# Kernel tuning notes

Measured on AMD Instinct MI355X. Metric: run time of the kernel, lower is better.

Reference implementation:

```python
import jax, jax.numpy as jnp
import numpy as np

EMBED = 1024
HEADS = 16
HEAD_DIM = EMBED // HEADS
B, S = 2, 2048


def setup_inputs() -> dict:
    key = jax.random.key(0)
    ks = jax.random.split(key, 11)
    sc = 1.0 / np.sqrt(EMBED)
    d = {
        'query': jax.random.normal(ks[0], (B, S, EMBED), jnp.float32),
        'key':   jax.random.normal(ks[1], (B, S, EMBED), jnp.float32),
        'value': jax.random.normal(ks[2], (B, S, EMBED), jnp.float32),
        'Wq': jax.random.normal(ks[3], (EMBED, EMBED), jnp.float32) * sc,
        'bq': jnp.zeros((EMBED,), jnp.float32),
        'Wk': jax.random.normal(ks[4], (EMBED, EMBED), jnp.float32) * sc,
        'bk': jnp.zeros((EMBED,), jnp.float32),
        'Wv': jax.random.normal(ks[5], (EMBED, EMBED), jnp.float32) * sc,
        'bv': jnp.zeros((EMBED,), jnp.float32),
        'Wo': jax.random.normal(ks[6], (EMBED, EMBED), jnp.float32) * sc,
        'bo': jnp.zeros((EMBED,), jnp.float32),
    }
    return d


def _split_heads(x):
    b, s, _ = x.shape
    return x.reshape(b, s, HEADS, HEAD_DIM).transpose(0, 2, 1, 3)  # [B,H,S,D]


def reference(query, key, value, Wq, bq, Wk, bk, Wv, bv, Wo, bo):
    # nn.Linear: y = x @ W^T + b
    q = _split_heads(query @ Wq.T + bq)
    k = _split_heads(key @ Wk.T + bk)
    v = _split_heads(value @ Wv.T + bv)
    scale = 1.0 / np.sqrt(HEAD_DIM).astype(np.float32)
    attn = jnp.einsum('bhqd,bhkd->bhqk', q, k) * scale  # [B,H,S,S]
    attn = jax.nn.softmax(attn, axis=-1)
    out = jnp.einsum('bhqk,bhkd->bhqd', attn, v)
    out = out.transpose(0, 2, 1, 3).reshape(query.shape[0], -1, EMBED)
    return out @ Wo.T + bo
```

## Files before the change

### kernel.cpp

```cpp
#include <hip/hip_runtime.h>

typedef _Float16 f16;
typedef __fp16   fp16n2 __attribute__((ext_vector_type(2)));
typedef _Float16 f16x8 __attribute__((ext_vector_type(8)));
typedef float    f32x2 __attribute__((ext_vector_type(2)));
typedef float    f32x4 __attribute__((ext_vector_type(4)));
typedef float    f32x16 __attribute__((ext_vector_type(16)));
typedef int      i32x2 __attribute__((ext_vector_type(2)));
typedef unsigned short u16;
typedef unsigned long long u64;

#define B_ 2
#define S_ 2048
#define E_ 1024
#define H_ 16
#define D_ 64
#define M_ (B_*S_)
#define LOG2E 1.44269504088896340736f

__device__ __forceinline__ f32x4 mfma16(f16x8 a, f16x8 b, f32x4 c) {
  return __builtin_amdgcn_mfma_f32_16x16x32_f16(a, b, c, 0, 0, 0);
}
__device__ __forceinline__ f32x16 mfma32(f16x8 a, f16x8 b, f32x16 c) {
  return __builtin_amdgcn_mfma_f32_32x32x16_f16(a, b, c, 0, 0, 0);
}

__device__ __forceinline__ void gload_lds16(const void* g, void* l) {
  __builtin_amdgcn_global_load_lds(
      (const __attribute__((address_space(1))) unsigned int*)g,
      (__attribute__((address_space(3))) unsigned int*)l, 16, 0, 0);
}

__device__ __forceinline__ int pkrtz(float a, float b) {
  union { fp16n2 h; int i; } u;
  u.h = __builtin_amdgcn_cvt_pkrtz(a, b);
  return u.i;
}

__device__ __forceinline__ u16 f16bits(float x) {
  union { f16 h; u16 u; } c; c.h = (f16)x; return c.u;
}

__device__ __forceinline__ f32x16 Z16() {
  f32x16 z = {0.f,0.f,0.f,0.f,0.f,0.f,0.f,0.f,0.f,0.f,0.f,0.f,0.f,0.f,0.f,0.f};
  return z;
}

__device__ __forceinline__ f32x2 pr2(const f32x16& v, int j) {
  return (f32x2){v[2 * j], v[2 * j + 1]};
}

__global__ __launch_bounds__(256) void cast_all(
    const float* __restrict__ q, const float* __restrict__ k, const float* __restrict__ v,
    const float* __restrict__ wq, const float* __restrict__ wk,
    const float* __restrict__ wv, const float* __restrict__ wo,
    f16* __restrict__ xq, f16* __restrict__ xk, f16* __restrict__ xv,
    f16* __restrict__ wqh, f16* __restrict__ wkh, f16* __restrict__ wvh,
    f16* __restrict__ woh) {
  int i = blockIdx.x * 256 + threadIdx.x;
  const float* src; f16* dst; int off;
  if (i < 3 * 524288) {
    int seg = i >> 19; off = i & 524287;
    src = seg == 0 ? q : seg == 1 ? k : v;
    dst = seg == 0 ? xq : seg == 1 ? xk : xv;
  } else {
    int j = i - 3 * 524288;
    int seg = j >> 17; off = j & 131071;
    src = seg == 0 ? wq : seg == 1 ? wk : seg == 2 ? wv : wo;
    dst = seg == 0 ? wqh : seg == 1 ? wkh : seg == 2 ? wvh : woh;
  }
  const float4* s = (const float4*)src;
  float4 a = s[off * 2], b = s[off * 2 + 1];
  f16x8 o = { (f16)a.x, (f16)a.y, (f16)a.z, (f16)a.w,
              (f16)b.x, (f16)b.y, (f16)b.z, (f16)b.w };
  *(f16x8*)&dst[(size_t)off * 8] = o;
}

__device__ __forceinline__ void gemm_core128(const f16* __restrict__ A,
                                             const f16* __restrict__ Bm,
                                             int m0, int n0,
                                             f32x4 (&acc)[4][2]) {
  __shared__ f16 Al[2][128 * 32];
  __shared__ f16 Bl[2][128 * 32];
  const int tid = threadIdx.x;
  const int w = tid >> 6, lane = tid & 63, lg = lane >> 4, ll = lane & 15;
  const int wr = (w & 1) * 64, wc = (w >> 1) * 32;

  const f32x4 zero4 = {0.f, 0.f, 0.f, 0.f};
#pragma unroll
  for (int m = 0; m < 4; ++m) { acc[m][0] = zero4; acc[m][1] = zero4; }

  const int lgs = (lg ^ ((ll >> 1) & 3)) * 8;
  const int row = tid >> 2;
  const int c8  = ((tid & 3) ^ ((tid >> 3) & 3)) * 8;

  for (int k0 = 0; k0 < 1024; k0 += 64) {
    __syncthreads();
#pragma unroll
    for (int ks = 0; ks < 2; ++ks) {
      gload_lds16(&A [(size_t)(m0 + row) * 1024 + k0 + ks * 32 + c8], &Al[ks][tid * 8]);
      gload_lds16(&Bm[(size_t)(n0 + row) * 1024 + k0 + ks * 32 + c8], &Bl[ks][tid * 8]);
    }
    __syncthreads();

#pragma unroll
    for (int ks = 0; ks < 2; ++ks) {
      f16x8 af[4], bf[2];
#pragma unroll
      for (int m = 0; m < 4; ++m) af[m] = *(const f16x8*)&Al[ks][(wr + m * 16 + ll) * 32 + lgs];
#pragma unroll
      for (int n = 0; n < 2; ++n) bf[n] = *(const f16x8*)&Bl[ks][(wc + n * 16 + ll) * 32 + lgs];
#pragma unroll
      for (int m = 0; m < 4; ++m)
#pragma unroll
        for (int n = 0; n < 2; ++n) acc[m][n] = mfma16(af[m], bf[n], acc[m][n]);
    }
  }
}

__global__ __launch_bounds__(512, 4) void gemm_qkv(
    const f16* __restrict__ Xq, const f16* __restrict__ Xk, const f16* __restrict__ Xv,
    const f16* __restrict__ Wq, const f16* __restrict__ Wk, const f16* __restrict__ Wv,
    const float* __restrict__ bq, const float* __restrict__ bk, const float* __restrict__ bv,
    f16* __restrict__ Qb, f16* __restrict__ Kb, f16* __restrict__ Vt) {
  const int z = blockIdx.z;
  const f16*   A    = (z == 0) ? Xq : (z == 1) ? Xk : Xv;
  const f16*   Bm   = (z == 0) ? Wq : (z == 1) ? Wk : Wv;
  const float* bias = (z == 0) ? bq : (z == 1) ? bk : bv;
  const float scale = (z == 0) ? (0.125f * LOG2E) : 1.0f;
  const int m0 = blockIdx.x * 128, n0 = blockIdx.y * 128;

  f32x4 acc[4][2];
  gemm_core128(A, Bm, m0, n0, acc);

  const int tid = threadIdx.x;
  const int w = tid >> 6, lane = tid & 63, lg = lane >> 4, ll = lane & 15;
  const int wr = (w & 1) * 64, wc = (w >> 1) * 32;

  if (z == 2) {
#pragma unroll
    for (int m = 0; m < 4; ++m)
#pragma unroll
      for (int n = 0; n < 2; ++n) {
        int col = n0 + wc + n * 16 + ll;
        float bv_ = bias[col];
        int h = col >> 6, d = col & 63;
        int rowb = m0 + wr + m * 16 + lg * 4;
        int b = rowb >> 11, s = rowb & 2047;
        u64 pk = (u64)f16bits(acc[m][n][0] + bv_)
               | ((u64)f16bits(acc[m][n][1] + bv_) << 16)
               | ((u64)f16bits(acc[m][n][2] + bv_) << 32)
               | ((u64)f16bits(acc[m][n][3] + bv_) << 48);
        *(u64*)&Vt[(((size_t)(b * H_ + h)) * D_ + d) * S_ + s] = pk;
      }
    return;
  }

  f16* dst = (z == 0) ? Qb : Kb;
#pragma unroll
  for (int m = 0; m < 4; ++m)
#pragma unroll
    for (int n = 0; n < 2; ++n) {
      int col = n0 + wc + n * 16 + ll;
      float bv_ = bias[col];
      int h = col >> 6, d = col & 63;
#pragma unroll
      for (int r = 0; r < 4; ++r) {
        int row = m0 + wr + m * 16 + lg * 4 + r;
        int b = row >> 11, s = row & 2047;
        float v = (acc[m][n][r] + bv_) * scale;
        dst[(((size_t)(b * H_ + h)) * S_ + s) * D_ + d] = (f16)v;
      }
    }
}

__device__ __forceinline__ void gemm_core64(const f16* __restrict__ A,
                                            const f16* __restrict__ Bm,
                                            int m0, int n0,
                                            f32x4 (&acc)[4][2]) {
  __shared__ f16 Al[2][128 * 32];
  __shared__ f16 Bl[2][64 * 32];
  const int tid = threadIdx.x;
  const int w = tid >> 6, lane = tid & 63, lg = lane >> 4, ll = lane & 15;
  const int wr = (w >> 1) * 64, wc = (w & 1) * 32;

  const f32x4 zero4 = {0.f, 0.f, 0.f, 0.f};
#pragma unroll
  for (int m = 0; m < 4; ++m) { acc[m][0] = zero4; acc[m][1] = zero4; }

  const int lgs = (lg ^ ((ll >> 1) & 3)) * 8;

  for (int k0 = 0; k0 < 1024; k0 += 64) {
    __syncthreads();
#pragma unroll
    for (int ks = 0; ks < 2; ++ks) {
#pragma unroll
      for (int it = 0; it < 2; ++it) {
        int chunk = it * 256 + tid;
        int row = chunk >> 2;
        int c8 = ((chunk & 3) ^ ((chunk >> 3) & 3)) * 8;
        gload_lds16(&A[(size_t)(m0 + row) * 1024 + k0 + ks * 32 + c8],
                    &Al[ks][chunk * 8]);
      }
      {
        int chunk = tid;
        int row = chunk >> 2;
        int c8 = ((chunk & 3) ^ ((chunk >> 3) & 3)) * 8;
        gload_lds16(&Bm[(size_t)(n0 + row) * 1024 + k0 + ks * 32 + c8],
                    &Bl[ks][chunk * 8]);
      }
    }
    __syncthreads();

#pragma unroll
    for (int ks = 0; ks < 2; ++ks) {
      f16x8 af[4], bf[2];
#pragma unroll
      for (int m = 0; m < 4; ++m) af[m] = *(const f16x8*)&Al[ks][(wr + m * 16 + ll) * 32 + lgs];
#pragma unroll
      for (int n = 0; n < 2; ++n) bf[n] = *(const f16x8*)&Bl[ks][(wc + n * 16 + ll) * 32 + lgs];
#pragma unroll
      for (int m = 0; m < 4; ++m)
#pragma unroll
        for (int n = 0; n < 2; ++n) acc[m][n] = mfma16(af[m], bf[n], acc[m][n]);
    }
  }
}

__global__ __launch_bounds__(256) void gemm_out(const f16* __restrict__ A,
                                                const f16* __restrict__ W,
                                                const float* __restrict__ bias,
                                                float* __restrict__ out) {
  const int m0 = blockIdx.x * 128, n0 = blockIdx.y * 64;
  f32x4 acc[4][2];
  gemm_core64(A, W, m0, n0, acc);

  const int tid = threadIdx.x;
  const int w = tid >> 6, lane = tid & 63, lg = lane >> 4, ll = lane & 15;
  const int wr = (w >> 1) * 64, wc = (w & 1) * 32;
#pragma unroll
  for (int m = 0; m < 4; ++m)
#pragma unroll
    for (int n = 0; n < 2; ++n) {
      int col = n0 + wc + n * 16 + ll;
      float bv_ = bias[col];
#pragma unroll
      for (int r = 0; r < 4; ++r) {
        int row = m0 + wr + m * 16 + lg * 4 + r;
        out[(size_t)row * 1024 + col] = acc[m][n][r] + bv_;
      }
    }
}

__global__ __launch_bounds__(512, 4) void attn_fwd(const f16* __restrict__ Q,
                                                   const f16* __restrict__ K,
                                                   const f16* __restrict__ VT,
                                                   f16* __restrict__ O) {
  const int qt = blockIdx.x, bh = blockIdx.y;
  const int tid = threadIdx.x;
  const int w = tid >> 6, lane = tid & 63;
  const int ql = lane & 31, hi = lane >> 5;
  const int qsub = w & 3, kvh = w >> 2;

  __shared__ __align__(16) char smem[32768];
  char* hb = smem + kvh * 16384;

  const f16* Qb = Q  + (size_t)bh * S_ * D_;
  const f16* Kb = K  + (size_t)bh * S_ * D_ + (size_t)(kvh * 1024) * D_;
  const f16* Vb = VT + (size_t)bh * D_ * S_ + kvh * 1024;
  const int q0 = qt * 128 + qsub * 32;

  f16x8 qf[4];
#pragma unroll
  for (int ks = 0; ks < 4; ++ks)
    qf[ks] = *(const f16x8*)&Qb[(size_t)(q0 + ql) * 64 + ks * 16 + hi * 8];

  f32x16 accO[2];
  accO[0] = Z16(); accO[1] = Z16();
  float l_r = 0.f;

  const int seg = w & 3;
  const int lr = lane >> 3;
  const int lc = lane & 7;
  const int cs = lc ^ lr;

#pragma unroll 1
  for (int kt = 0; kt < 16; ++kt) {
    __syncthreads();
#pragma unroll
    for (int i_ = 0; i_ < 2; ++i_) {
      int r_ = seg * 16 + i_ * 8 + lr;
      gload_lds16(&Kb[(size_t)(kt * 64 + r_) * 64 + cs * 8],
                  hb + seg * 2048 + i_ * 1024);
      gload_lds16(&Vb[(size_t)r_ * S_ + kt * 64 + cs * 8],
                  hb + 8192 + seg * 2048 + i_ * 1024);
    }
    __syncthreads();

    char* KlB = hb;
    char* VlB = hb + 8192;

    f32x16 accS[2];
    __builtin_amdgcn_s_setprio(1);
#pragma unroll
    for (int c = 0; c < 2; ++c) {
      int row = c * 32 + ql;
      int rb = row * 128, sw = (row & 7) << 4;
      f16x8 kf0 = *(const f16x8*)(KlB + rb + ((hi * 16) ^ sw));
      accS[c] = mfma32(kf0, qf[0], Z16());
#pragma unroll
      for (int ks = 1; ks < 4; ++ks) {
        f16x8 kf = *(const f16x8*)(KlB + rb + (((ks * 2 + hi) * 16) ^ sw));
        accS[c] = mfma32(kf, qf[ks], accS[c]);
      }
    }
    __builtin_amdgcn_s_setprio(0);

    f32x2 rs2 = {0.f, 0.f};
#pragma unroll
    for (int c = 0; c < 2; ++c)
#pragma unroll
      for (int j = 0; j < 8; ++j) {
        float p0 = __builtin_amdgcn_exp2f(accS[c][2 * j]);
        float p1 = __builtin_amdgcn_exp2f(accS[c][2 * j + 1]);
        accS[c][2 * j]     = p0;
        accS[c][2 * j + 1] = p1;
        rs2 += (f32x2){p0, p1};
      }
    l_r += rs2.x + rs2.y;

#pragma unroll
    for (int c = 0; c < 2; ++c)
#pragma unroll
      for (int s = 0; s < 2; ++s) {
        int b0 = s * 8;
        int a0 = pkrtz(accS[c][b0 + 0], accS[c][b0 + 1]);
        int a1 = pkrtz(accS[c][b0 + 2], accS[c][b0 + 3]);
        int a2 = pkrtz(accS[c][b0 + 4], accS[c][b0 + 5]);
        int a3 = pkrtz(accS[c][b0 + 6], accS[c][b0 + 7]);
        i32x2 r02 = __builtin_amdgcn_permlane32_swap(a0, a2, false, false);
        i32x2 r13 = __builtin_amdgcn_permlane32_swap(a1, a3, false, false);
        union { int i[4]; f16x8 h; } pf;
        pf.i[0] = r02.x; pf.i[1] = r13.x; pf.i[2] = r02.y; pf.i[3] = r13.y;
        int kvb = c * 64 + s * 32 + hi * 16;
        __builtin_amdgcn_s_setprio(1);
#pragma unroll
        for (int dc = 0; dc < 2; ++dc) {
          int dr = dc * 32 + ql;
          f16x8 vf = *(const f16x8*)(VlB + dr * 128 + (kvb ^ ((dr & 7) << 4)));
          accO[dc] = mfma32(vf, pf.h, accO[dc]);
        }
        __builtin_amdgcn_s_setprio(0);
      }
  }

  l_r += __shfl_xor(l_r, 32);

  __syncthreads();
  float* lB = (float*)smem;
  f16* Ep = (f16*)(smem + 1024);
  if (kvh == 1) {
    if (hi == 0) lB[qsub * 32 + ql] = l_r;
#pragma unroll
    for (int dc = 0; dc < 2; ++dc)
#pragma unroll
      for (int g = 0; g < 4; ++g) {
        int d0 = g * 8 + hi * 4 + dc * 32;
        u64 pk = (u64)f16bits(accO[dc][g * 4 + 0])
               | ((u64)f16bits(accO[dc][g * 4 + 1]) << 16)
               | ((u64)f16bits(accO[dc][g * 4 + 2]) << 32)
               | ((u64)f16bits(accO[dc][g * 4 + 3]) << 48);
        *(u64*)&Ep[(qsub * 32 + ql) * 68 + d0] = pk;
      }
  }
  __syncthreads();
  if (kvh == 0) {
    float inv = 1.0f / (l_r + lB[qsub * 32 + ql]);
#pragma unroll
    for (int dc = 0; dc < 2; ++dc)
#pragma unroll
      for (int g = 0; g < 4; ++g) {
        int d0 = g * 8 + hi * 4 + dc * 32;
        union { u64 v; f16 h[4]; } o2;
        o2.v = *(const u64*)&Ep[(qsub * 32 + ql) * 68 + d0];
        u64 pk = (u64)f16bits((accO[dc][g * 4 + 0] + (float)o2.h[0]) * inv)
               | ((u64)f16bits((accO[dc][g * 4 + 1] + (float)o2.h[1]) * inv) << 16)
               | ((u64)f16bits((accO[dc][g * 4 + 2] + (float)o2.h[2]) * inv) << 32)
               | ((u64)f16bits((accO[dc][g * 4 + 3] + (float)o2.h[3]) * inv) << 48);
        *(u64*)&Ep[(qsub * 32 + ql) * 68 + d0] = pk;
      }
  }
  __syncthreads();
  const int b = bh >> 4, h = bh & 15;
#pragma unroll
  for (int pass = 0; pass < 2; ++pass) {
    int idx = pass * 512 + tid;
    int row = idx >> 3, cx = idx & 7;
    f16x8 v = *(const f16x8*)&Ep[row * 68 + cx * 8];
    *(f16x8*)&O[((size_t)(b * S_ + qt * 128 + row)) * E_ + h * 64 + cx * 8] = v;
  }
}

extern "C" void kernel_launch(void* const* d_in, const int* in_sizes, int n_in,
                              void* d_out, int out_size, void* d_ws, size_t ws_size,
                              hipStream_t stream) {
  (void)in_sizes; (void)n_in; (void)out_size; (void)ws_size;
  const float* q  = (const float*)d_in[0];
  const float* k  = (const float*)d_in[1];
  const float* v  = (const float*)d_in[2];
  const float* Wq = (const float*)d_in[3];
  const float* bq = (const float*)d_in[4];
  const float* Wk = (const float*)d_in[5];
  const float* bk = (const float*)d_in[6];
  const float* Wv = (const float*)d_in[7];
  const float* bv = (const float*)d_in[8];
  const float* Wo = (const float*)d_in[9];
  const float* bo = (const float*)d_in[10];
  float* out = (float*)d_out;

  f16* ws  = (f16*)d_ws;
  f16* Xq  = ws;
  f16* Xk  = Xq  + (size_t)M_ * E_;
  f16* Xv  = Xk  + (size_t)M_ * E_;
  f16* Wqh = Xv  + (size_t)M_ * E_;
  f16* Wkh = Wqh + (size_t)E_ * E_;
  f16* Wvh = Wkh + (size_t)E_ * E_;
  f16* Woh = Wvh + (size_t)E_ * E_;
  f16* Qb  = Woh + (size_t)E_ * E_;
  f16* Kb  = Qb  + (size_t)M_ * E_;
  f16* VTb = Kb  + (size_t)M_ * E_;
  f16* AO  = Xq;

  cast_all<<<8192, 256, 0, stream>>>(q, k, v, Wq, Wk, Wv, Wo,
                                     Xq, Xk, Xv, Wqh, Wkh, Wvh, Woh);

  gemm_qkv<<<dim3(M_ / 128, E_ / 128, 3), 512, 0, stream>>>(
      Xq, Xk, Xv, Wqh, Wkh, Wvh, bq, bk, bv, Qb, Kb, VTb);

  attn_fwd<<<dim3(S_ / 128, B_ * H_), 512, 0, stream>>>(Qb, Kb, VTb, AO);

  gemm_out<<<dim3(M_ / 128, E_ / 64), 256, 0, stream>>>(AO, Woh, bo, out);
}
```

Before: 114.7 us.

## Split attention KV range across four wave groups per block instead of two

```diff
diff --git a/kernel.cpp b/kernel.cpp
--- a/kernel.cpp
+++ b/kernel.cpp
@@ -252,22 +252,22 @@
     }
 }
 
-__global__ __launch_bounds__(512, 4) void attn_fwd(const f16* __restrict__ Q,
-                                                   const f16* __restrict__ K,
-                                                   const f16* __restrict__ VT,
-                                                   f16* __restrict__ O) {
+__global__ __launch_bounds__(1024, 4) void attn_fwd(const f16* __restrict__ Q,
+                                                    const f16* __restrict__ K,
+                                                    const f16* __restrict__ VT,
+                                                    f16* __restrict__ O) {
   const int qt = blockIdx.x, bh = blockIdx.y;
   const int tid = threadIdx.x;
   const int w = tid >> 6, lane = tid & 63;
   const int ql = lane & 31, hi = lane >> 5;
   const int qsub = w & 3, kvh = w >> 2;
 
-  __shared__ __align__(16) char smem[32768];
+  __shared__ __align__(16) char smem[65536];
   char* hb = smem + kvh * 16384;
 
   const f16* Qb = Q  + (size_t)bh * S_ * D_;
-  const f16* Kb = K  + (size_t)bh * S_ * D_ + (size_t)(kvh * 1024) * D_;
-  const f16* Vb = VT + (size_t)bh * D_ * S_ + kvh * 1024;
+  const f16* Kb = K  + (size_t)bh * S_ * D_ + (size_t)(kvh * 512) * D_;
+  const f16* Vb = VT + (size_t)bh * D_ * S_ + kvh * 512;
   const int q0 = qt * 128 + qsub * 32;
 
   f16x8 qf[4];
@@ -285,7 +285,7 @@
   const int cs = lc ^ lr;
 
 #pragma unroll 1
-  for (int kt = 0; kt < 16; ++kt) {
+  for (int kt = 0; kt < 8; ++kt) {
     __syncthreads();
 #pragma unroll
     for (int i_ = 0; i_ < 2; ++i_) {
@@ -358,9 +358,10 @@
 
   __syncthreads();
   float* lB = (float*)smem;
-  f16* Ep = (f16*)(smem + 1024);
-  if (kvh == 1) {
-    if (hi == 0) lB[qsub * 32 + ql] = l_r;
+  const int qrow = qsub * 32 + ql;
+  if (kvh > 0) {
+    f16* EpH = (f16*)(smem + 2048 + (kvh - 1) * 17408);
+    if (hi == 0) lB[(kvh - 1) * 128 + qrow] = l_r;
 #pragma unroll
     for (int dc = 0; dc < 2; ++dc)
 #pragma unroll
@@ -370,33 +371,37 @@
                | ((u64)f16bits(accO[dc][g * 4 + 1]) << 16)
                | ((u64)f16bits(accO[dc][g * 4 + 2]) << 32)
                | ((u64)f16bits(accO[dc][g * 4 + 3]) << 48);
-        *(u64*)&Ep[(qsub * 32 + ql) * 68 + d0] = pk;
+        *(u64*)&EpH[qrow * 68 + d0] = pk;
       }
   }
   __syncthreads();
+  f16* Ep0 = (f16*)(smem + 2048);
   if (kvh == 0) {
-    float inv = 1.0f / (l_r + lB[qsub * 32 + ql]);
+    float inv = 1.0f / (l_r + lB[qrow] + lB[128 + qrow] + lB[256 + qrow]);
 #pragma unroll
     for (int dc = 0; dc < 2; ++dc)
 #pragma unroll
       for (int g = 0; g < 4; ++g) {
         int d0 = g * 8 + hi * 4 + dc * 32;
-        union { u64 v; f16 h[4]; } o2;
-        o2.v = *(const u64*)&Ep[(qsub * 32 + ql) * 68 + d0];
-        u64 pk = (u64)f16bits((accO[dc][g * 4 + 0] + (float)o2.h[0]) * inv)
-               | ((u64)f16bits((accO[dc][g * 4 + 1] + (float)o2.h[1]) * inv) << 16)
-               | ((u64)f16bits((accO[dc][g * 4 + 2] + (float)o2.h[2]) * inv) << 32)
-               | ((u64)f16bits((accO[dc][g * 4 + 3] + (float)o2.h[3]) * inv) << 48);
-        *(u64*)&Ep[(qsub * 32 + ql) * 68 + d0] = pk;
+        union { u64 v; f16 h[4]; } p1, p2, p3;
+        p1.v = *(const u64*)(smem + 2048 +             qrow * 136 + d0 * 2);
+        p2.v = *(const u64*)(smem + 2048 + 17408 +     qrow * 136 + d0 * 2);
+        p3.v = *(const u64*)(smem + 2048 + 2 * 17408 + qrow * 136 + d0 * 2);
+        u64 pk = 0;
+#pragma unroll
+        for (int r = 0; r < 4; ++r) {
+          float s = accO[dc][g * 4 + r] + (float)p1.h[r] + (float)p2.h[r] + (float)p3.h[r];
+          pk |= (u64)f16bits(s * inv) << (16 * r);
+        }
+        *(u64*)&Ep0[qrow * 68 + d0] = pk;
       }
   }
   __syncthreads();
   const int b = bh >> 4, h = bh & 15;
-#pragma unroll
-  for (int pass = 0; pass < 2; ++pass) {
-    int idx = pass * 512 + tid;
+  {
+    int idx = tid;
     int row = idx >> 3, cx = idx & 7;
-    f16x8 v = *(const f16x8*)&Ep[row * 68 + cx * 8];
+    f16x8 v = *(const f16x8*)&Ep0[row * 68 + cx * 8];
     *(f16x8*)&O[((size_t)(b * S_ + qt * 128 + row)) * E_ + h * 64 + cx * 8] = v;
   }
 }
@@ -437,7 +442,7 @@
   gemm_qkv<<<dim3(M_ / 128, E_ / 128, 3), 512, 0, stream>>>(
       Xq, Xk, Xv, Wqh, Wkh, Wvh, bq, bk, bv, Qb, Kb, VTb);
 
-  attn_fwd<<<dim3(S_ / 128, B_ * H_), 512, 0, stream>>>(Qb, Kb, VTb, AO);
+  attn_fwd<<<dim3(S_ / 128, B_ * H_), 1024, 0, stream>>>(Qb, Kb, VTb, AO);
 
   gemm_out<<<dim3(M_ / 128, E_ / 64), 256, 0, stream>>>(AO, Woh, bo, out);
 }
```

Measured after the change: 125.8 us. 9.6% more time.
